# Performance work log

Hardware: AMD Instinct MI355X
Metric: run time of the kernel (lower is better)

Reference implementation:

```python
import jax, jax.numpy as jnp
import numpy as np

N, D, V = 4096, 2048, 50257
IGNORE_INDEX = -100


def setup_inputs() -> dict:
    key = jax.random.key(0)
    k1, k2, k3 = jax.random.split(key, 3)
    x = jax.random.normal(k1, (N, D), dtype=jnp.float32)
    # lm_head.weight is [V, D]; the fused op receives weight.T -> [D, V]
    weight = jax.random.normal(k2, (D, V), dtype=jnp.float32) * (1.0 / np.sqrt(D))
    target = jax.random.randint(k3, (N,), 0, V, dtype=jnp.int64)
    return {"x": x, "weight": weight, "target": target}


def reference(x, weight, target):
    # Fused linear + cross-entropy (reduction='sum'), matching the Helion kernel math:
    # logits accumulated in fp32, online logsumexp == plain stable logsumexp.
    logits = jnp.matmul(x, weight, preferred_element_type=jnp.float32)  # [N, V] fp32
    lse = jax.nn.logsumexp(logits, axis=-1)                              # [N]
    tgt_idx = jnp.clip(target, 0, V - 1)                                 # safe gather
    target_logits = jnp.take_along_axis(logits, tgt_idx[:, None], axis=-1)[:, 0]
    per_token_loss = lse - target_logits                                 # [N]
    mask = (target != IGNORE_INDEX).astype(per_token_loss.dtype)
    ce_loss = jnp.sum(per_token_loss * mask)                             # reduction='sum'
    return ce_loss
```

## Files before the change

kernel.cpp:

```cpp
#include <hip/hip_runtime.h>
#include <hip/hip_bf16.h>
#include <stdint.h>

#define N_TOK 4096
#define DDIM  2048
#define VOCAB 50257
#define IGNORE_INDEX (-100)

#define BM 128
#define BN 128
#define BK 64
#define NT (DDIM / BK)
#define VCHUNKS ((VOCAB + BN - 1) / BN)
#define VP (VCHUNKS * BN)
#define ROW_TILES (N_TOK / BM)
#define GRID_MAIN (VCHUNKS * ROW_TILES)

#define W_SCALE 32.0f
#define W_INV   0.03125f
#define SCALE_1 0x7F7F7F7FU

typedef float f32x4  __attribute__((ext_vector_type(4)));
typedef float f32x16 __attribute__((ext_vector_type(16)));
typedef int   i32x4  __attribute__((ext_vector_type(4)));
typedef int   i32x8  __attribute__((ext_vector_type(8)));

__device__ __forceinline__ uint32_t pack2bf(float a, float b) {
  uint32_t ua = __float_as_uint(a);
  uint32_t ub = __float_as_uint(b);
  uint32_t ra = (ua + 0x7fffu + ((ua >> 16) & 1u)) >> 16;
  uint32_t rb = (ub + 0x7fffu + ((ub >> 16) & 1u)) & 0xffff0000u;
  return (ra & 0xffffu) | rb;
}

__device__ __forceinline__ uint32_t f32_to_e4m3(float f) {
  uint32_t u = __float_as_uint(f);
  uint32_t s = (u >> 24) & 0x80u;
  float a = fabsf(f);
  if (a >= 448.f) return s | 0x7Eu;
  if (a >= 0.015625f) {
    uint32_t m = __float_as_uint(a);
    m += 0x7FFFFu + ((m >> 20) & 1u);
    uint32_t e = (m >> 23) - 120u;
    return s | (e << 3) | ((m >> 20) & 7u);
  }
  uint32_t m = (uint32_t)rintf(a * 512.f);
  return s | m;
}

__device__ __forceinline__ void gload_lds16(const void* g, void* l) {
  __builtin_amdgcn_global_load_lds(
      (const __attribute__((address_space(1))) uint32_t*)g,
      (__attribute__((address_space(3))) uint32_t*)l, 16, 0, 0);
}


__global__ __launch_bounds__(256) void convert_x8(const float* __restrict__ x,
                                                  uint8_t* __restrict__ xp) {
  int t = blockIdx.x * 256 + threadIdx.x;
  const int n = t >> 7;
  const int q = t & 127;
  const float4* src = (const float4*)(x + (size_t)n * DDIM + q * 16);
  uint32_t u[4];
  #pragma unroll
  for (int g = 0; g < 4; ++g) {
    float4 f = src[g];
    u[g] = f32_to_e4m3(f.x) | (f32_to_e4m3(f.y) << 8) |
           (f32_to_e4m3(f.z) << 16) | (f32_to_e4m3(f.w) << 24);
  }
  const int T = q >> 2, rem = q & 3;
  const int hi = rem >> 1, p = rem & 1;
  const int tb = n >> 5, r5 = n & 31;
  const int l = hi * 32 + r5;
  uint8_t* dst = xp + (((size_t)tb * NT + T) * 2 + p) * 1024 + l * 16;
  *(uint4*)dst = make_uint4(u[0], u[1], u[2], u[3]);
}

__global__ __launch_bounds__(256) void transpose_w8(const float* __restrict__ w,
                                                    uint8_t* __restrict__ w8) {
  __shared__ float t[64][68];
  const int vb = blockIdx.x * 128;
  const int kb = blockIdx.y * 64;
  const int tid = threadIdx.x;

  const int fq = tid & 31;
  const int r8 = tid >> 5;
  if (vb + 128 <= VOCAB) {
    #pragma unroll
    for (int i = 0; i < 8; ++i) {
      int kl = r8 + i * 8;
      float4 f = *(const float4*)(w + (size_t)(kb + kl) * VOCAB + vb + fq * 4);
      *(float4*)&t[kl][fq * 4] = make_float4(f.x * W_SCALE, f.y * W_SCALE,
                                             f.z * W_SCALE, f.w * W_SCALE);
    }
  } else {
    #pragma unroll
    for (int i = 0; i < 8; ++i) {
      int kl = r8 + i * 8;
      #pragma unroll
      for (int c = 0; c < 4; ++c) {
        int v = vb + fq * 4 + c;
        t[kl][fq * 4 + c] =
            (v < VOCAB) ? w[(size_t)(kb + kl) * VOCAB + v] * W_SCALE : 0.f;
      }
    }
  }
  __syncthreads();

  const int vl = tid >> 1, half = tid & 1;
  uint32_t u[8];
  #pragma unroll
  for (int g = 0; g < 8; ++g) {
    u[g] = 0;
    #pragma unroll
    for (int j = 0; j < 4; ++j)
      u[g] |= f32_to_e4m3(t[half * 32 + g * 4 + j][vl]) << (8 * j);
  }
  uint8_t* dst = w8 + (size_t)(vb + vl) * DDIM + kb + half * 32;
  *(uint4*)dst = make_uint4(u[0], u[1], u[2], u[3]);
  *(uint4*)(dst + 16) = make_uint4(u[4], u[5], u[6], u[7]);
}

struct Bregs { i32x4 v[2][2]; };

__global__ __launch_bounds__(256, 3) void lmhead_main(
    const uint8_t* __restrict__ w8, const uint8_t* __restrict__ xp,
    const int* __restrict__ tgt,
    float2* __restrict__ partial, float* __restrict__ tlogit)
{
  __shared__ char lds[16384];
  __shared__ float2 stats[2][BM];

  const int bid = blockIdx.x;
  const int v = bid >> 5;
  const int r = bid & 31;
  const int v0 = v * BN;
  const int m0 = r * BM;
  const int tid = threadIdx.x;
  const int lane = tid & 63;
  const int wid = tid >> 6;
  const int wn = wid >> 1, wm = wid & 1;

  f32x16 acc[2][2];
  #pragma unroll
  for (int i = 0; i < 2; ++i)
    #pragma unroll
    for (int j = 0; j < 2; ++j) acc[i][j] = (f32x16)0.f;

  const int jj = lane >> 3;
  const int lu_s = (lane & 7) ^ jj;
  const int srow = 2 * jj + (lu_s >> 2);
  const int sk = (lu_s & 3) * 16;
  const uint8_t* wsrc = w8 + (size_t)(v0 + srow) * DDIM + sk;

  const int r5 = lane & 31, hi = lane >> 5;
  const int j7 = (r5 >> 1) & 7;
  const int lu0 = ((r5 & 1) << 2) | (hi << 1);
  const int rdoff = (r5 >> 1) * 128 + ((lu0 ^ j7) << 4);
  const int aoff0 = wn * 4096 + rdoff;

  const int tb0 = (m0 >> 5) + wm * 2;
  const uint8_t* xb0 = xp + ((size_t)tb0 * NT) * 2048 + lane * 16;
  const uint8_t* xb1 = xp + ((size_t)(tb0 + 1) * NT) * 2048 + lane * 16;

  auto stageA = [&](int T, int s) {
    char* Al = lds + s * 8192;
    const size_t ko = (size_t)T * BK;
    #pragma unroll
    for (int i = 0; i < 2; ++i) {
      int c = wid * 2 + i;
      gload_lds16(wsrc + (size_t)c * 16 * DDIM + ko, Al + c * 1024);
    }
  };
  auto loadB = [&](Bregs& B, int T) {
    const uint8_t* p0 = xb0 + (size_t)T * 2048;
    const uint8_t* p1 = xb1 + (size_t)T * 2048;
    B.v[0][0] = *(const i32x4*)(p0);
    B.v[0][1] = *(const i32x4*)(p0 + 1024);
    B.v[1][0] = *(const i32x4*)(p1);
    B.v[1][1] = *(const i32x4*)(p1 + 1024);
  };
  auto computeT = [&](const char* Al, const Bregs& B) {
    i32x8 bv[2];
    #pragma unroll
    for (int bj = 0; bj < 2; ++bj)
      bv[bj] = __builtin_shufflevector(B.v[bj][0], B.v[bj][1],
                                       0, 1, 2, 3, 4, 5, 6, 7);
    #pragma unroll
    for (int bi = 0; bi < 2; ++bi) {
      i32x4 a0 = *(const i32x4*)(Al + (aoff0 + bi * 2048));
      i32x4 a1 = *(const i32x4*)(Al + ((aoff0 ^ 16) + bi * 2048));
      i32x8 av = __builtin_shufflevector(a0, a1, 0, 1, 2, 3, 4, 5, 6, 7);
      #pragma unroll
      for (int bj = 0; bj < 2; ++bj)
        acc[bi][bj] = __builtin_amdgcn_mfma_scale_f32_32x32x64_f8f6f4(
            av, bv[bj], acc[bi][bj], 0 , 0 ,
            0, SCALE_1, 0, SCALE_1);
    }
  };

  Bregs B0, B1;
  stageA(0, 0);
  loadB(B0, 0);
  __syncthreads();

  for (int t = 0; t < NT; t += 2) {
    if (t + 1 < NT) { stageA(t + 1, 1); loadB(B1, t + 1); }
    computeT(lds, B0);
    __syncthreads();
    if (t + 2 < NT) { stageA(t + 2, 0); loadB(B0, t + 2); }
    computeT(lds + 8192, B1);
    __syncthreads();
  }

  #pragma unroll
  for (int bj = 0; bj < 2; ++bj) {
    const int m_g = m0 + wm * 64 + bj * 32 + r5;
    float vmax = -INFINITY;
    #pragma unroll
    for (int bi = 0; bi < 2; ++bi) {
      #pragma unroll
      for (int rg = 0; rg < 16; ++rg) {
        int n_g = v0 + wn * 64 + bi * 32 + (rg & 3) + 8 * (rg >> 2) + 4 * hi;
        if (n_g < VOCAB) vmax = fmaxf(vmax, acc[bi][bj][rg] * W_INV);
      }
    }
    vmax = fmaxf(vmax, __shfl_xor(vmax, 32, 64));
    float ssum = 0.f;
    const int t = tgt[m_g];
    #pragma unroll
    for (int bi = 0; bi < 2; ++bi) {
      #pragma unroll
      for (int rg = 0; rg < 16; ++rg) {
        int n_g = v0 + wn * 64 + bi * 32 + (rg & 3) + 8 * (rg >> 2) + 4 * hi;
        float val = acc[bi][bj][rg] * W_INV;
        if (n_g < VOCAB) ssum += __expf(val - vmax);
        if (n_g == t) tlogit[m_g] = val;
      }
    }
    ssum += __shfl_xor(ssum, 32, 64);
    if (hi == 0) stats[wn][wm * 64 + bj * 32 + r5] = make_float2(vmax, ssum);
  }
  __syncthreads();
  if (tid < BM) {
    float2 a = stats[0][tid], b = stats[1][tid];
    float M = fmaxf(a.x, b.x);
    float S = a.y * __expf(a.x - M) + b.y * __expf(b.x - M);
    partial[(size_t)(m0 + tid) * VCHUNKS + v] = make_float2(M, S);
  }
}

typedef short bf16x8 __attribute__((ext_vector_type(8)));

__global__ __launch_bounds__(256, 2) void lmhead_partial_fb(
    const float* __restrict__ x, const float* __restrict__ w,
    const int* __restrict__ tgt,
    float2* __restrict__ partial, float* __restrict__ tlogit)
{
  __shared__ uint4 xs[BM * 64 * 2 / 16];
  __shared__ uint4 wtl[BN * 64 * 2 / 16];
  __shared__ float2 stats[2][BM];

  const int bid = blockIdx.x;
  const int v = bid >> 5;
  const int r = bid & 31;
  const int v0 = v * BN;
  const int m0 = r * BM;
  const int tid = threadIdx.x;
  const int lane = tid & 63;
  const int wid = tid >> 6;
  const int wn = wid >> 1, wm = wid & 1;
  const int lr = lane & 15, lk = lane >> 4;

  f32x4 acc[4][4];
  #pragma unroll
  for (int i = 0; i < 4; ++i)
    #pragma unroll
    for (int j = 0; j < 4; ++j) acc[i][j] = (f32x4)0.f;

  char* xsb = (char*)xs;
  char* wtb = (char*)wtl;

  for (int kt = 0; kt < DDIM / 64; ++kt) {
    const int k0 = kt * 64;
    __syncthreads();
    #pragma unroll
    for (int i = 0; i < 4; ++i) {
      int t = tid + i * 256;
      int m = t >> 3, kg = t & 7;
      const float* gp = x + (size_t)(m0 + m) * DDIM + k0 + kg * 8;
      float4 f0 = *(const float4*)gp;
      float4 f1 = *(const float4*)(gp + 4);
      uint4 pk;
      pk.x = pack2bf(f0.x, f0.y); pk.y = pack2bf(f0.z, f0.w);
      pk.z = pack2bf(f1.x, f1.y); pk.w = pack2bf(f1.z, f1.w);
      int byte = (m * 128 + kg * 16) ^ ((m & 7) << 4);
      *(uint4*)(xsb + byte) = pk;
    }
    #pragma unroll
    for (int i = 0; i < 4; ++i) {
      int t = tid + i * 256;
      int n = t & 127, kg = t >> 7;
      int col = v0 + n;
      float f[8];
      if (col < VOCAB) {
        const float* gp = w + (size_t)(k0 + kg * 8) * VOCAB + col;
        #pragma unroll
        for (int kk = 0; kk < 8; ++kk) f[kk] = gp[(size_t)kk * VOCAB];
      } else {
        #pragma unroll
        for (int kk = 0; kk < 8; ++kk) f[kk] = 0.f;
      }
      uint4 pk;
      pk.x = pack2bf(f[0], f[1]); pk.y = pack2bf(f[2], f[3]);
      pk.z = pack2bf(f[4], f[5]); pk.w = pack2bf(f[6], f[7]);
      int byte = (n * 128 + kg * 16) ^ ((n & 7) << 4);
      *(uint4*)(wtb + byte) = pk;
    }
    __syncthreads();
    #pragma unroll
    for (int ks = 0; ks < 2; ++ks) {
      bf16x8 af[4], bfr[4];
      #pragma unroll
      for (int bi = 0; bi < 4; ++bi) {
        int row = wn * 64 + bi * 16 + lr;
        int byte = (row * 128 + ks * 64 + lk * 16) ^ ((row & 7) << 4);
        af[bi] = *(const bf16x8*)(wtb + byte);
      }
      #pragma unroll
      for (int bj = 0; bj < 4; ++bj) {
        int row = wm * 64 + bj * 16 + lr;
        int byte = (row * 128 + ks * 64 + lk * 16) ^ ((row & 7) << 4);
        bfr[bj] = *(const bf16x8*)(xsb + byte);
      }
      #pragma unroll
      for (int bi = 0; bi < 4; ++bi)
        #pragma unroll
        for (int bj = 0; bj < 4; ++bj)
          acc[bi][bj] = __builtin_amdgcn_mfma_f32_16x16x32_bf16(
              af[bi], bfr[bj], acc[bi][bj], 0, 0, 0);
    }
  }

  #pragma unroll
  for (int bj = 0; bj < 4; ++bj) {
    const int m_g = m0 + wm * 64 + bj * 16 + lr;
    float vmax = -INFINITY;
    #pragma unroll
    for (int bi = 0; bi < 4; ++bi)
      #pragma unroll
      for (int rg = 0; rg < 4; ++rg) {
        int n_g = v0 + wn * 64 + bi * 16 + lk * 4 + rg;
        if (n_g < VOCAB) vmax = fmaxf(vmax, acc[bi][bj][rg]);
      }
    vmax = fmaxf(vmax, __shfl_xor(vmax, 16, 64));
    vmax = fmaxf(vmax, __shfl_xor(vmax, 32, 64));
    float ssum = 0.f;
    const int t = tgt[m_g];
    #pragma unroll
    for (int bi = 0; bi < 4; ++bi)
      #pragma unroll
      for (int rg = 0; rg < 4; ++rg) {
        int n_g = v0 + wn * 64 + bi * 16 + lk * 4 + rg;
        float val = acc[bi][bj][rg];
        if (n_g < VOCAB) ssum += __expf(val - vmax);
        if (n_g == t) tlogit[m_g] = val;
      }
    ssum += __shfl_xor(ssum, 16, 64);
    ssum += __shfl_xor(ssum, 32, 64);
    if (lk == 0) stats[wn][wm * 64 + bj * 16 + lr] = make_float2(vmax, ssum);
  }
  __syncthreads();
  if (tid < BM) {
    float2 a = stats[0][tid], b = stats[1][tid];
    float M = fmaxf(a.x, b.x);
    float S = a.y * __expf(a.x - M) + b.y * __expf(b.x - M);
    partial[(size_t)(m0 + tid) * VCHUNKS + v] = make_float2(M, S);
  }
}

__device__ __forceinline__ void lse_merge(float& m, float& s, float M, float S) {
  if (S > 0.f) {
    if (M > m) { s = s * __expf(m - M) + S; m = M; }
    else       { s += S * __expf(M - m); }
  }
}

__global__ void lmhead_reduce(const float2* __restrict__ partial,
                              const float* __restrict__ tlogit,
                              const int* __restrict__ tgt,
                              float* __restrict__ out)
{
  const int wid = threadIdx.x >> 6;
  const int lane = threadIdx.x & 63;
  const int row = blockIdx.x * 4 + wid;
  float m = -INFINITY, s = 0.f;
  for (int c = lane; c < VCHUNKS; c += 64) {
    float2 p = partial[(size_t)row * VCHUNKS + c];
    lse_merge(m, s, p.x, p.y);
  }
  #pragma unroll
  for (int off = 1; off < 64; off <<= 1) {
    float M = __shfl_xor(m, off, 64);
    float S = __shfl_xor(s, off, 64);
    lse_merge(m, s, M, S);
  }
  if (lane == 0) {
    int t = tgt[row];
    if (t != IGNORE_INDEX) {
      float loss = m + __logf(s) - tlogit[row];
      atomicAdd(out, loss);
    }
  }
}

extern "C" void kernel_launch(void* const* d_in, const int* in_sizes, int n_in,
                              void* d_out, int out_size, void* d_ws, size_t ws_size,
                              hipStream_t stream) {
  const float* x = (const float*)d_in[0];
  const float* w = (const float*)d_in[1];
  const int* tgt = (const int*)d_in[2];
  float* out = (float*)d_out;

  const size_t w8_bytes = (size_t)VP * DDIM;
  const size_t x8_bytes = (size_t)N_TOK * DDIM;
  const size_t part_bytes = (size_t)N_TOK * VCHUNKS * 8;
  const size_t tl_bytes = (size_t)N_TOK * 4;
  const size_t need = w8_bytes + x8_bytes + part_bytes + tl_bytes;

  hipMemsetAsync(d_out, 0, sizeof(float), stream);

  if (ws_size >= need) {
    uint8_t* w8 = (uint8_t*)d_ws;
    uint8_t* xp = (uint8_t*)d_ws + w8_bytes;
    float2* partial = (float2*)((char*)d_ws + w8_bytes + x8_bytes);
    float* tlogit = (float*)((char*)d_ws + w8_bytes + x8_bytes + part_bytes);

    convert_x8<<<dim3(N_TOK * DDIM / 16 / 256), 256, 0, stream>>>(x, xp);
    transpose_w8<<<dim3(VP / 128, DDIM / 64), 256, 0, stream>>>(w, w8);
    lmhead_main<<<dim3(GRID_MAIN), 256, 0, stream>>>(w8, xp, tgt, partial, tlogit);
    lmhead_reduce<<<dim3(N_TOK / 4), 256, 0, stream>>>(partial, tlogit, tgt, out);
  } else {
    float2* partial = (float2*)d_ws;
    float* tlogit = (float*)((char*)d_ws + part_bytes);
    lmhead_partial_fb<<<dim3(GRID_MAIN), 256, 0, stream>>>(x, w, tgt, partial, tlogit);
    lmhead_reduce<<<dim3(N_TOK / 4), 256, 0, stream>>>(partial, tlogit, tgt, out);
  }
}
```

Baseline: 639.1 us.

## Prepack weights into MFMA fragment layout and load A operands directly to registers

The weight transpose kernel now writes fp8 weights in the same per-lane fragment-packed layout already used for x, so the main kernel can load both operands directly from global memory into registers. This removes the LDS staging buffer, the LDS reads, and the block-wide barriers from the K loop. The cost is that each wave now fetches its own A fragments from global or L2 instead of sharing them through LDS across waves, which raises global or L2 traffic. It also puts more register pressure on the double-buffered operand sets.

```diff
diff --git a/kernel.cpp b/kernel.cpp
--- a/kernel.cpp
+++ b/kernel.cpp
@@ -48,12 +48,6 @@
   return s | m;
 }
 
-__device__ __forceinline__ void gload_lds16(const void* g, void* l) {
-  __builtin_amdgcn_global_load_lds(
-      (const __attribute__((address_space(1))) uint32_t*)g,
-      (__attribute__((address_space(3))) uint32_t*)l, 16, 0, 0);
-}
-
 
 __global__ __launch_bounds__(256) void convert_x8(const float* __restrict__ x,
                                                   uint8_t* __restrict__ xp) {
@@ -76,11 +70,12 @@
   *(uint4*)dst = make_uint4(u[0], u[1], u[2], u[3]);
 }
 
-__global__ __launch_bounds__(256) void transpose_w8(const float* __restrict__ w,
-                                                    uint8_t* __restrict__ w8) {
+__global__ __launch_bounds__(256) void transpose_w8p(const float* __restrict__ w,
+                                                     uint8_t* __restrict__ w8p) {
   __shared__ float t[64][68];
   const int vb = blockIdx.x * 128;
-  const int kb = blockIdx.y * 64;
+  const int T  = blockIdx.y;
+  const int kb = T * 64;
   const int tid = threadIdx.x;
 
   const int fq = tid & 31;
@@ -107,28 +102,30 @@
   }
   __syncthreads();
 
-  const int vl = tid >> 1, half = tid & 1;
+  const int vl = tid >> 1, hi = tid & 1;
+  const int vb32 = (vb >> 5) + (vl >> 5);
+  const int r5 = vl & 31;
+  const int l = hi * 32 + r5;
   uint32_t u[8];
   #pragma unroll
   for (int g = 0; g < 8; ++g) {
     u[g] = 0;
     #pragma unroll
     for (int j = 0; j < 4; ++j)
-      u[g] |= f32_to_e4m3(t[half * 32 + g * 4 + j][vl]) << (8 * j);
-  }
-  uint8_t* dst = w8 + (size_t)(vb + vl) * DDIM + kb + half * 32;
-  *(uint4*)dst = make_uint4(u[0], u[1], u[2], u[3]);
-  *(uint4*)(dst + 16) = make_uint4(u[4], u[5], u[6], u[7]);
-}
-
-struct Bregs { i32x4 v[2][2]; };
+      u[g] |= f32_to_e4m3(t[hi * 32 + g * 4 + j][vl]) << (8 * j);
+  }
+  uint8_t* base = w8p + (((size_t)vb32 * NT + T) * 2) * 1024 + l * 16;
+  *(uint4*)base = make_uint4(u[0], u[1], u[2], u[3]);
+  *(uint4*)(base + 1024) = make_uint4(u[4], u[5], u[6], u[7]);
+}
+
+struct Oregs { i32x4 v[2][2]; };
 
 __global__ __launch_bounds__(256, 3) void lmhead_main(
-    const uint8_t* __restrict__ w8, const uint8_t* __restrict__ xp,
+    const uint8_t* __restrict__ w8p, const uint8_t* __restrict__ xp,
     const int* __restrict__ tgt,
     float2* __restrict__ partial, float* __restrict__ tlogit)
 {
-  __shared__ char lds[16384];
   __shared__ float2 stats[2][BM];
 
   const int bid = blockIdx.x;
@@ -140,6 +137,7 @@
   const int lane = tid & 63;
   const int wid = tid >> 6;
   const int wn = wid >> 1, wm = wid & 1;
+  const int r5 = lane & 31, hi = lane >> 5;
 
   f32x16 acc[2][2];
   #pragma unroll
@@ -147,32 +145,22 @@
     #pragma unroll
     for (int j = 0; j < 2; ++j) acc[i][j] = (f32x16)0.f;
 
-  const int jj = lane >> 3;
-  const int lu_s = (lane & 7) ^ jj;
-  const int srow = 2 * jj + (lu_s >> 2);
-  const int sk = (lu_s & 3) * 16;
-  const uint8_t* wsrc = w8 + (size_t)(v0 + srow) * DDIM + sk;
-
-  const int r5 = lane & 31, hi = lane >> 5;
-  const int j7 = (r5 >> 1) & 7;
-  const int lu0 = ((r5 & 1) << 2) | (hi << 1);
-  const int rdoff = (r5 >> 1) * 128 + ((lu0 ^ j7) << 4);
-  const int aoff0 = wn * 4096 + rdoff;
-
+  const int ab0 = (v0 >> 5) + wn * 2;
+  const uint8_t* wa0 = w8p + ((size_t)ab0 * NT) * 2048 + lane * 16;
+  const uint8_t* wa1 = w8p + ((size_t)(ab0 + 1) * NT) * 2048 + lane * 16;
   const int tb0 = (m0 >> 5) + wm * 2;
   const uint8_t* xb0 = xp + ((size_t)tb0 * NT) * 2048 + lane * 16;
   const uint8_t* xb1 = xp + ((size_t)(tb0 + 1) * NT) * 2048 + lane * 16;
 
-  auto stageA = [&](int T, int s) {
-    char* Al = lds + s * 8192;
-    const size_t ko = (size_t)T * BK;
-    #pragma unroll
-    for (int i = 0; i < 2; ++i) {
-      int c = wid * 2 + i;
-      gload_lds16(wsrc + (size_t)c * 16 * DDIM + ko, Al + c * 1024);
-    }
+  auto loadA = [&](Oregs& A, int T) {
+    const uint8_t* p0 = wa0 + (size_t)T * 2048;
+    const uint8_t* p1 = wa1 + (size_t)T * 2048;
+    A.v[0][0] = *(const i32x4*)(p0);
+    A.v[0][1] = *(const i32x4*)(p0 + 1024);
+    A.v[1][0] = *(const i32x4*)(p1);
+    A.v[1][1] = *(const i32x4*)(p1 + 1024);
   };
-  auto loadB = [&](Bregs& B, int T) {
+  auto loadB = [&](Oregs& B, int T) {
     const uint8_t* p0 = xb0 + (size_t)T * 2048;
     const uint8_t* p1 = xb1 + (size_t)T * 2048;
     B.v[0][0] = *(const i32x4*)(p0);
@@ -180,37 +168,29 @@
     B.v[1][0] = *(const i32x4*)(p1);
     B.v[1][1] = *(const i32x4*)(p1 + 1024);
   };
-  auto computeT = [&](const char* Al, const Bregs& B) {
-    i32x8 bv[2];
-    #pragma unroll
-    for (int bj = 0; bj < 2; ++bj)
-      bv[bj] = __builtin_shufflevector(B.v[bj][0], B.v[bj][1],
-                                       0, 1, 2, 3, 4, 5, 6, 7);
-    #pragma unroll
-    for (int bi = 0; bi < 2; ++bi) {
-      i32x4 a0 = *(const i32x4*)(Al + (aoff0 + bi * 2048));
-      i32x4 a1 = *(const i32x4*)(Al + ((aoff0 ^ 16) + bi * 2048));
-      i32x8 av = __builtin_shufflevector(a0, a1, 0, 1, 2, 3, 4, 5, 6, 7);
+  auto computeT = [&](const Oregs& A, const Oregs& B) {
+    i32x8 av[2], bv[2];
+    #pragma unroll
+    for (int k = 0; k < 2; ++k) {
+      av[k] = __builtin_shufflevector(A.v[k][0], A.v[k][1], 0, 1, 2, 3, 4, 5, 6, 7);
+      bv[k] = __builtin_shufflevector(B.v[k][0], B.v[k][1], 0, 1, 2, 3, 4, 5, 6, 7);
+    }
+    #pragma unroll
+    for (int bi = 0; bi < 2; ++bi)
       #pragma unroll
       for (int bj = 0; bj < 2; ++bj)
         acc[bi][bj] = __builtin_amdgcn_mfma_scale_f32_32x32x64_f8f6f4(
-            av, bv[bj], acc[bi][bj], 0 , 0 ,
+            av[bi], bv[bj], acc[bi][bj], 0 , 0 ,
             0, SCALE_1, 0, SCALE_1);
-    }
   };
 
-  Bregs B0, B1;
-  stageA(0, 0);
-  loadB(B0, 0);
-  __syncthreads();
-
+  Oregs A0, A1, B0, B1;
+  loadA(A0, 0); loadB(B0, 0);
   for (int t = 0; t < NT; t += 2) {
-    if (t + 1 < NT) { stageA(t + 1, 1); loadB(B1, t + 1); }
-    computeT(lds, B0);
-    __syncthreads();
-    if (t + 2 < NT) { stageA(t + 2, 0); loadB(B0, t + 2); }
-    computeT(lds + 8192, B1);
-    __syncthreads();
+    if (t + 1 < NT) { loadA(A1, t + 1); loadB(B1, t + 1); }
+    computeT(A0, B0);
+    if (t + 2 < NT) { loadA(A0, t + 2); loadB(B0, t + 2); }
+    computeT(A1, B1);
   }
 
   #pragma unroll
@@ -431,14 +411,14 @@
   hipMemsetAsync(d_out, 0, sizeof(float), stream);
 
   if (ws_size >= need) {
-    uint8_t* w8 = (uint8_t*)d_ws;
+    uint8_t* w8p = (uint8_t*)d_ws;
     uint8_t* xp = (uint8_t*)d_ws + w8_bytes;
     float2* partial = (float2*)((char*)d_ws + w8_bytes + x8_bytes);
     float* tlogit = (float*)((char*)d_ws + w8_bytes + x8_bytes + part_bytes);
 
     convert_x8<<<dim3(N_TOK * DDIM / 16 / 256), 256, 0, stream>>>(x, xp);
-    transpose_w8<<<dim3(VP / 128, DDIM / 64), 256, 0, stream>>>(w, w8);
-    lmhead_main<<<dim3(GRID_MAIN), 256, 0, stream>>>(w8, xp, tgt, partial, tlogit);
+    transpose_w8p<<<dim3(VP / 128, DDIM / 64), 256, 0, stream>>>(w, w8p);
+    lmhead_main<<<dim3(GRID_MAIN), 256, 0, stream>>>(w8p, xp, tgt, partial, tlogit);
     lmhead_reduce<<<dim3(N_TOK / 4), 256, 0, stream>>>(partial, tlogit, tgt, out);
   } else {
     float2* partial = (float2*)d_ws;
```

Result: slower. 693.6 us (+8.5%).
